# Optimization experiments

Measured on AMD Instinct MI355X. Metric: run time of the kernel, lower is better.

## Reference

```python
import jax, jax.numpy as jnp
import numpy as np

B, P, C = 128, 8732, 21          # batch, num_priors (SSD300), num_classes incl. background
TOP_K = 200
VAR0, VAR1 = 0.1, 0.2            # SSD prior variances
CONF_THRESH = 0.01
NMS_THRESH = 0.45


def setup_inputs() -> dict:
    key = jax.random.key(0)
    k1, k2, k3, k4 = jax.random.split(key, 4)
    loc_data = jax.random.normal(k1, (B, P, 4), jnp.float32)
    conf_data = jax.random.normal(k2, (B * P, C), jnp.float32)
    # priors: (cx, cy, w, h) in [0,1], positive widths/heights
    cxy = jax.random.uniform(k3, (P, 2), jnp.float32)
    wh = jax.random.uniform(k4, (P, 2), jnp.float32, minval=0.02, maxval=0.3)
    prior_data = jnp.concatenate([cxy, wh], axis=-1)
    return {"loc_data": loc_data, "conf_data": conf_data, "prior_data": prior_data}


def _decode(loc, priors):
    # loc: [B,P,4], priors: [P,4] (cx,cy,w,h) -> corner boxes [B,P,4]
    xy = priors[:, :2] + loc[..., :2] * VAR0 * priors[:, 2:]
    wh = priors[:, 2:] * jnp.exp(loc[..., 2:] * VAR1)
    return jnp.concatenate([xy - wh * 0.5, xy + wh * 0.5], axis=-1)


def _nms_single(boxes, scores, idxs):
    # boxes [P,4] corners, scores [P] (-1 where below conf_thresh), idxs [P] int class ids
    x1, y1, x2, y2 = boxes[:, 0], boxes[:, 1], boxes[:, 2], boxes[:, 3]
    areas = (x2 - x1) * (y2 - y1)

    def body(s, _):
        i = jnp.argmax(s)          # highest remaining score
        si = s[i]
        valid = si > 0.0
        bi = boxes[i]
        # IoU of bi against all boxes
        ix1 = jnp.maximum(bi[0], x1)
        iy1 = jnp.maximum(bi[1], y1)
        ix2 = jnp.minimum(bi[2], x2)
        iy2 = jnp.minimum(bi[3], y2)
        inter = jnp.maximum(ix2 - ix1, 0.0) * jnp.maximum(iy2 - iy1, 0.0)
        area_i = (bi[2] - bi[0]) * (bi[3] - bi[1])
        iou = inter / (area_i + areas - inter)
        # class-aware (batched) NMS: only suppress same-class boxes; also kills i itself (iou=1)
        suppress = (iou > NMS_THRESH) & (idxs == idxs[i])
        s_new = jnp.where(suppress, -1.0, s)
        row = jnp.where(
            valid,
            jnp.concatenate([bi, si[None], idxs[i].astype(jnp.float32)[None]]),
            jnp.zeros(6, dtype=boxes.dtype),
        )
        return s_new, row

    _, rows = jax.lax.scan(body, scores, None, length=TOP_K)
    return rows  # [TOP_K, 6] = (x1,y1,x2,y2,score,class)


def reference(loc_data, conf_data, prior_data):
    # softmax over classes, drop background, per-prior best fg class
    conf = jax.nn.softmax(conf_data, axis=-1)[:, 1:].reshape(B, P, C - 1)
    scores = conf.max(axis=-1)           # [B,P]
    cls = jnp.argmax(conf, axis=-1)      # [B,P] fg class id (0..C-2)
    boxes = _decode(loc_data, prior_data)  # [B,P,4]
    masked = jnp.where(scores > CONF_THRESH, scores, -1.0)
    return jax.vmap(_nms_single)(boxes, masked, cls)  # [B, TOP_K, 6]
```

## Files before the change

kernel.cpp:

```cpp
#include <hip/hip_runtime.h>


typedef unsigned long long u64;

#define BATCH 128
#define NPRIOR 8732
#define NCLS 21
#define TOPK 200
#define T 1024
#define TARGET 256
#define CAP 384
#define NBIN 4096
#define KW 6

__device__ __forceinline__ double exp_fast(double x) {
  const double LOG2E = 1.4426950408889634;
  const double LN2_HI = 6.93147180369123816490e-01;
  const double LN2_LO = 1.90821492927058770002e-10;
  double n = rint(x * LOG2E);
  double r = fma(-n, LN2_HI, x);
  r = fma(-n, LN2_LO, r);
  double p = 2.505210838544172e-08;
  p = fma(p, r, 2.755731922398589e-07);
  p = fma(p, r, 2.7557319223985893e-06);
  p = fma(p, r, 2.48015873015873e-05);
  p = fma(p, r, 1.984126984126984e-04);
  p = fma(p, r, 1.388888888888889e-03);
  p = fma(p, r, 8.333333333333333e-03);
  p = fma(p, r, 4.1666666666666664e-02);
  p = fma(p, r, 1.6666666666666666e-01);
  p = fma(p, r, 0.5);
  p = fma(p, r, 1.0);
  p = fma(p, r, 1.0);
  return ldexp(p, (int)n);
}

__global__ __launch_bounds__(256) void prep_kernel(
    const float* __restrict__ conf, u64* __restrict__ keys) {
  __shared__ __align__(16) float srow[256 * NCLS];
  const int tid = threadIdx.x;
  const long long R0 = (long long)blockIdx.x * 256;
  const float4* src = (const float4*)(conf + R0 * NCLS);
  float4* dst = (float4*)srow;
  for (int k = tid; k < 1344; k += 256) dst[k] = src[k];
  __syncthreads();

  const float* row = srow + tid * NCLS;
  float m = row[0];
#pragma unroll
  for (int j = 1; j < NCLS; ++j) m = fmaxf(m, row[j]);
  float sum = __expf(row[0] - m);
  float bestr = row[1];
  float beste = __expf(row[1] - m);
  sum += beste;
  int bi = 1;
#pragma unroll
  for (int j = 2; j < NCLS; ++j) {
    float rv = row[j];
    float ej = __expf(rv - m);
    sum += ej;
    if (rv > bestr) { bestr = rv; bi = j; beste = ej; }
  }
  float score = __fdividef(beste, sum);

  const long long r = R0 + tid;
  const int p = (int)(r % NPRIOR);
  u64 key = 0ULL;
  if (score > 0.01f) {
    key = ((u64)__float_as_uint(score) << 32) |
          ((u64)(16383 - p) << 10) | (u64)(bi - 1);
  }
  keys[r] = key;
}

__device__ __forceinline__ void radix_cut(const int* hist, int tid, int tcap,
                                          int* wtot, int* cut) {
  if (tid == 0) cut[2] = 0;
  const int base = tid * 4;
  const int cs = hist[base] + hist[base + 1] + hist[base + 2] + hist[base + 3];
  const int lane = tid & 63;
  int suf = cs;
#pragma unroll
  for (int off = 1; off < 64; off <<= 1) {
    int v = __shfl_down(suf, off);
    if (lane + off < 64) suf += v;
  }
  if (lane == 0) wtot[tid >> 6] = suf;
  __syncthreads();
  if (tid < 16) {
    int v = wtot[tid];
    int s = v;
#pragma unroll
    for (int off = 1; off < 16; off <<= 1) {
      int o = __shfl_down(s, off);
      if (tid + off < 16) s += o;
    }
    if (tid == 0) wtot[16] = s;
    wtot[tid] = s - v;
  }
  __syncthreads();
  const int total = wtot[16];
  if (total > 0) {
    const int target = total < tcap ? total : tcap;
    const int S = suf + wtot[tid >> 6];
    const int Snext = S - cs;
    if (S >= target && Snext < target) {
      int acc = Snext;
      for (int bn = base + 3; bn >= base; --bn) {
        acc += hist[bn];
        if (acc >= target) {
          cut[0] = bn; cut[1] = acc - hist[bn]; cut[2] = acc;
          break;
        }
      }
    }
  }
  __syncthreads();
}

__global__ __launch_bounds__(T) void nms_kernel(
    const float* __restrict__ loc, const float* __restrict__ conf,
    const float* __restrict__ prior, const u64* __restrict__ keys,
    float* __restrict__ out) {
  __shared__ u64 Ks[NPRIOR];
  __shared__ __align__(16) char pool[53248];
  __shared__ int wtot[17];
  __shared__ int cut1[3], cut2[3];
  __shared__ u64 Ash[KW], KFsh[KW], ACCsh[KW];
  __shared__ float4 abox[TOPK];
  __shared__ float aar[TOPK];
  __shared__ int acl[TOPK];
  __shared__ int sh_cnt, sh_nA;
  __shared__ u64 sh_ub;

  const int tid = threadIdx.x;
  const int b = blockIdx.x;
  const float* confb = conf + (long long)b * (NPRIOR * NCLS);
  const float4* loc4 = ((const float4*)loc) + (long long)b * NPRIOR;
  const float4* pr4 = (const float4*)prior;
  float* outb = out + (long long)b * (TOPK * 6);

  for (int i = tid; i < NPRIOR; i += T) Ks[i] = keys[(long long)b * NPRIOR + i];
  if (tid == 0) { sh_nA = 0; sh_ub = ~0ULL; }
  __syncthreads();

  int* hist = (int*)pool;
  u64* buf = (u64*)(pool + 16384);
  u64* ebuf = (u64*)(pool + 19456);
  u64* buf2 = (u64*)(pool + 22528);
  float4* cbox = (float4*)(pool + 25600);
  float* car = (float*)(pool + 31744);
  int* ccl = (int*)(pool + 33280);
  u64* KILL = (u64*)(pool + 34816);

  while (true) {
    for (int i = tid; i < NBIN; i += T) hist[i] = 0;
    __syncthreads();
    const u64 ub = sh_ub;
    for (int i = tid; i < NPRIOR; i += T) {
      u64 k = Ks[i];
      if (k && k < ub) atomicAdd(&hist[(int)((k >> 46) & 0xFFF)], 1);
    }
    __syncthreads();
    radix_cut(hist, tid, TARGET, wtot, cut1);
    const int total = wtot[16];
    int M = cut1[2];
    if (M == 0) break;
    const int c1 = cut1[0];
    const int baseA = cut1[1];
    const bool need2 = (M > CAP);
    int c2 = 0;
    if (need2) {
      for (int i = tid; i < NBIN; i += T) hist[i] = 0;
      __syncthreads();
      for (int i = tid; i < NPRIOR; i += T) {
        u64 k = Ks[i];
        if (k && k < ub && (int)((k >> 46) & 0xFFF) == c1)
          atomicAdd(&hist[(int)((k >> 34) & 0xFFF)], 1);
      }
      __syncthreads();
      const int tcap2 = (total < TARGET ? total : TARGET) - baseA;
      radix_cut(hist, tid, tcap2, wtot, cut2);
      c2 = cut2[0];
      M = baseA + cut2[2];
      if (M > CAP) {
        int Md = M - hist[c2];
        if (Md > 0) { M = Md; c2 = c2 + 1; } else { M = CAP; }
      }
    }
    if (tid == 0) {
      sh_cnt = 0;
      sh_ub = need2 ? (((u64)c1 << 46) + ((u64)c2 << 34)) : ((u64)c1 << 46);
    }
    __syncthreads();
    for (int i = tid; i < NPRIOR; i += T) {
      u64 k = Ks[i];
      bool psel = false;
      if (k && k < ub) {
        int b1 = (int)((k >> 46) & 0xFFF);
        psel = need2 ? (b1 > c1 || (b1 == c1 && (int)((k >> 34) & 0xFFF) >= c2))
                     : (b1 >= c1);
      }
      u64 mask = __ballot(psel ? 1 : 0);
      if (mask) {
        int lane = tid & 63;
        int leader = __ffsll((unsigned long long)mask) - 1;
        int bpos = 0;
        if (lane == leader) bpos = atomicAdd(&sh_cnt, __popcll(mask));
        bpos = __shfl(bpos, leader);
        if (psel) {
          int pos = bpos + __popcll(mask & ((1ULL << lane) - 1ULL));
          if (pos < CAP) buf[pos] = k;
        }
      }
    }
    __syncthreads();
    int Mr = sh_cnt;
    if (Mr > CAP) Mr = CAP;
    if (Mr == 0) break;
    if (tid < Mr) {
      u64 ak = buf[tid];
      int cl = (int)(ak & 0x1FULL);
      int p = 16383 - (int)((ak >> 10) & 0x3FFFULL);
      const float* crow = confb + (long long)p * NCLS;
      double m = (double)crow[0];
#pragma unroll
      for (int j = 1; j < NCLS; ++j) m = fmax(m, (double)crow[j]);
      double sum = 0.0, best = -1.0;
#pragma unroll
      for (int j = 0; j < NCLS; ++j) {
        double ej = exp_fast((double)crow[j] - m);
        sum += ej;
        if (j >= 1 && ej > best) best = ej;
      }
      double score = best / sum;
      u64 sb = (u64)__double_as_longlong(score);
      ebuf[tid] = ((sb >> 24) << 24) | ((u64)(16383 - p) << 10) | (u64)cl;
    }
    __syncthreads();
    if (tid < Mr) {
      u64 ka = ebuf[tid];
      int ra = 0;
      for (int i = 0; i < Mr; ++i) ra += (ebuf[i] > ka);
      buf2[ra] = ka;
    }
    if (tid < KW) { Ash[tid] = 0ULL; KFsh[tid] = 0ULL; }
    __syncthreads();
    const int nA0 = sh_nA;
    if (tid < Mr) {
      const int t = tid;
      u64 k = buf2[t];
      int cl = (int)(k & 0x1FULL);
      int p = 16383 - (int)((k >> 10) & 0x3FFFULL);
      float4 l = loc4[p];
      float4 pr = pr4[p];
      double cx = (double)pr.x + (double)l.x * 0.1 * (double)pr.z;
      double cy = (double)pr.y + (double)l.y * 0.1 * (double)pr.w;
      double w = (double)pr.z * exp_fast((double)l.z * 0.2);
      double h = (double)pr.w * exp_fast((double)l.w * 0.2);
      float x1 = (float)(cx - w * 0.5), y1 = (float)(cy - h * 0.5);
      float x2 = (float)(cx + w * 0.5), y2 = (float)(cy + h * 0.5);
      cbox[t] = make_float4(x1, y1, x2, y2);
      car[t] = (x2 - x1) * (y2 - y1);
      ccl[t] = cl;
    }
    __syncthreads();
    if (nA0 > 0 && tid < Mr) {
      const int t = tid;
      float4 my = cbox[t];
      float mar = car[t];
      int mcl = ccl[t];
      bool sup = false;
      for (int a = 0; a < nA0; ++a) {
        if (acl[a] == mcl) {
          float4 ab = abox[a];
          float ix1 = fmaxf(ab.x, my.x), iy1 = fmaxf(ab.y, my.y);
          float ix2 = fminf(ab.z, my.z), iy2 = fminf(ab.w, my.w);
          float inter = fmaxf(ix2 - ix1, 0.f) * fmaxf(iy2 - iy1, 0.f);
          if (inter > 0.45f * (aar[a] + mar - inter)) sup = true;
        }
      }
      if (sup) atomicOr(&Ash[t >> 6], 1ULL << (t & 63));
    }
    for (int idx = tid; idx < KW * 512; idx += T) {
      const int seg = idx >> 9;
      const int t = idx & 511;
      if (t < Mr) {
        const int i0 = seg * 64;
        int i1 = i0 + 64;
        if (i1 > Mr) i1 = Mr;
        u64 mm = 0ULL;
        if (i1 > t) {
          float4 my = cbox[t];
          float mar = car[t];
          int mcl = ccl[t];
          int is = (i0 > t + 1) ? i0 : (t + 1);
          for (int i = is; i < i1; ++i) {
            if (ccl[i] == mcl) {
              float4 cb = cbox[i];
              float ix1 = fmaxf(my.x, cb.x), iy1 = fmaxf(my.y, cb.y);
              float ix2 = fminf(my.z, cb.z), iy2 = fminf(my.w, cb.w);
              float inter = fmaxf(ix2 - ix1, 0.f) * fmaxf(iy2 - iy1, 0.f);
              if (inter > 0.45f * (mar + car[i] - inter))
                mm |= 1ULL << (i - i0);
            }
          }
        }
        KILL[t * KW + seg] = mm;
        if (mm) atomicOr(&KFsh[t >> 6], 1ULL << (t & 63));
      }
    }
    __syncthreads();
    if (tid < 64) {
      u64 A0, A1, A2, A3, A4, A5;
      {
        u64 v[KW];
#pragma unroll
        for (int w = 0; w < KW; ++w) {
          int rem = Mr - 64 * w;
          u64 vm = (rem >= 64) ? ~0ULL : (rem <= 0 ? 0ULL : ((1ULL << rem) - 1ULL));
          v[w] = vm & ~Ash[w];
        }
        A0 = v[0]; A1 = v[1]; A2 = v[2]; A3 = v[3]; A4 = v[4]; A5 = v[5];
      }
      u64 C0 = 0, C1 = 0, C2 = 0, C3 = 0, C4 = 0, C5 = 0;
      int nacc = nA0;
      bool full = false;
#define KILLUPD(cidx) do { const u64* kc = &KILL[(cidx) * KW];      \
      A0 &= ~kc[0]; A1 &= ~kc[1]; A2 &= ~kc[2];                     \
      A3 &= ~kc[3]; A4 &= ~kc[4]; A5 &= ~kc[5]; } while (0)
#define RESW(w, Aw, Cw) if (!full) {                                \
      const u64 KFw = KFsh[w];                                      \
      int lim = Mr - (w) * 64; if (lim > 64) lim = 64;              \
      for (int q = 0; q < lim; ++q) {                               \
        if ((Aw >> q) & 1ULL) {                                     \
          Cw |= 1ULL << q; ++nacc;                                  \
          if (nacc == TOPK) { full = true; break; }                 \
          if ((KFw >> q) & 1ULL) KILLUPD((w) * 64 + q);             \
        } } }
      RESW(0, A0, C0)
      RESW(1, A1, C1)
      RESW(2, A2, C2)
      RESW(3, A3, C3)
      RESW(4, A4, C4)
      RESW(5, A5, C5)
#undef RESW
#undef KILLUPD
      if (tid == 0) {
        ACCsh[0] = C0; ACCsh[1] = C1; ACCsh[2] = C2;
        ACCsh[3] = C3; ACCsh[4] = C4; ACCsh[5] = C5;
        sh_nA = nacc;
      }
    }
    __syncthreads();
    if (tid < Mr) {
      const int t = tid;
      const int w = t >> 6, q = t & 63;
      const u64 accw = ACCsh[w];
      if ((accw >> q) & 1ULL) {
        int rank = nA0;
#pragma unroll
        for (int w2 = 0; w2 < KW; ++w2)
          if (w2 < w) rank += __popcll(ACCsh[w2]);
        rank += __popcll(accw & ((q == 0) ? 0ULL : ((1ULL << q) - 1ULL)));
        float4 bx = cbox[t];
        float sc = (float)__longlong_as_double((long long)((buf2[t] >> 24) << 24));
        float* o = outb + rank * 6;
        o[0] = bx.x; o[1] = bx.y; o[2] = bx.z; o[3] = bx.w;
        o[4] = sc; o[5] = (float)ccl[t];
        abox[rank] = bx; aar[rank] = car[t]; acl[rank] = ccl[t];
      }
    }
    __syncthreads();
    if (sh_nA >= TOPK) break;
    if (total - Mr <= 0) break;
  }
  const int nAf = sh_nA;
  for (int i = nAf * 6 + tid; i < TOPK * 6; i += T) outb[i] = 0.0f;
}

extern "C" void kernel_launch(void* const* d_in, const int* in_sizes, int n_in,
                              void* d_out, int out_size, void* d_ws,
                              size_t ws_size, hipStream_t stream) {
  const float* loc = (const float*)d_in[0];
  const float* conf = (const float*)d_in[1];
  const float* prior = (const float*)d_in[2];
  float* out = (float*)d_out;

  u64* keys = (u64*)d_ws;

  const int nrows_blocks = (BATCH * NPRIOR) / 256;
  prep_kernel<<<nrows_blocks, 256, 0, stream>>>(conf, keys);
  nms_kernel<<<BATCH, T, 0, stream>>>(loc, conf, prior, keys, out);
}
```

Before: 211.2 us.

## Micro-optimize NMS kernel: bit-built exp scale, typed LDS arrays, unrolled rank loops

Replaces ldexp in the double exp polynomial with a multiply by a power of two built from raw bits. The untyped shared pool is split into separately typed shared arrays, and conf rows are loaded into registers before the softmax. The rank-by-count loop is unrolled by 8 and the pairwise IoU loop gets an unroll pragma. These target instruction overhead and load latency in the candidate scoring and suppression stages. The bit-built scale has no handling for out-of-range exponents, though the softmax inputs here stay small.

```diff
diff --git a/kernel.cpp b/kernel.cpp
--- a/kernel.cpp
+++ b/kernel.cpp
@@ -32,7 +32,8 @@
   p = fma(p, r, 0.5);
   p = fma(p, r, 1.0);
   p = fma(p, r, 1.0);
-  return ldexp(p, (int)n);
+  double scale = __longlong_as_double(((long long)(1023 + (int)n)) << 52);
+  return p * scale;
 }
 
 __global__ __launch_bounds__(256) void prep_kernel(
@@ -123,7 +124,14 @@
     const float* __restrict__ prior, const u64* __restrict__ keys,
     float* __restrict__ out) {
   __shared__ u64 Ks[NPRIOR];
-  __shared__ __align__(16) char pool[53248];
+  __shared__ int hist[NBIN];
+  __shared__ u64 buf[CAP];
+  __shared__ u64 ebuf[CAP];
+  __shared__ u64 buf2[CAP];
+  __shared__ float4 cbox[CAP];
+  __shared__ float car[CAP];
+  __shared__ int ccl[CAP];
+  __shared__ u64 KILL[CAP * KW];
   __shared__ int wtot[17];
   __shared__ int cut1[3], cut2[3];
   __shared__ u64 Ash[KW], KFsh[KW], ACCsh[KW];
@@ -143,15 +151,6 @@
   for (int i = tid; i < NPRIOR; i += T) Ks[i] = keys[(long long)b * NPRIOR + i];
   if (tid == 0) { sh_nA = 0; sh_ub = ~0ULL; }
   __syncthreads();
-
-  int* hist = (int*)pool;
-  u64* buf = (u64*)(pool + 16384);
-  u64* ebuf = (u64*)(pool + 19456);
-  u64* buf2 = (u64*)(pool + 22528);
-  float4* cbox = (float4*)(pool + 25600);
-  float* car = (float*)(pool + 31744);
-  int* ccl = (int*)(pool + 33280);
-  u64* KILL = (u64*)(pool + 34816);
 
   while (true) {
     for (int i = tid; i < NBIN; i += T) hist[i] = 0;
@@ -223,13 +222,16 @@
       int cl = (int)(ak & 0x1FULL);
       int p = 16383 - (int)((ak >> 10) & 0x3FFFULL);
       const float* crow = confb + (long long)p * NCLS;
-      double m = (double)crow[0];
-#pragma unroll
-      for (int j = 1; j < NCLS; ++j) m = fmax(m, (double)crow[j]);
+      float cr[NCLS];
+#pragma unroll
+      for (int j = 0; j < NCLS; ++j) cr[j] = crow[j];
+      double m = (double)cr[0];
+#pragma unroll
+      for (int j = 1; j < NCLS; ++j) m = fmax(m, (double)cr[j]);
       double sum = 0.0, best = -1.0;
 #pragma unroll
       for (int j = 0; j < NCLS; ++j) {
-        double ej = exp_fast((double)crow[j] - m);
+        double ej = exp_fast((double)cr[j] - m);
         sum += ej;
         if (j >= 1 && ej > best) best = ej;
       }
@@ -241,7 +243,14 @@
     if (tid < Mr) {
       u64 ka = ebuf[tid];
       int ra = 0;
-      for (int i = 0; i < Mr; ++i) ra += (ebuf[i] > ka);
+      int i = 0;
+      for (; i + 8 <= Mr; i += 8) {
+        u64 k0 = ebuf[i], k1 = ebuf[i + 1], k2 = ebuf[i + 2], k3 = ebuf[i + 3];
+        u64 k4 = ebuf[i + 4], k5 = ebuf[i + 5], k6 = ebuf[i + 6], k7 = ebuf[i + 7];
+        ra += (int)(k0 > ka) + (int)(k1 > ka) + (int)(k2 > ka) + (int)(k3 > ka) +
+              (int)(k4 > ka) + (int)(k5 > ka) + (int)(k6 > ka) + (int)(k7 > ka);
+      }
+      for (; i < Mr; ++i) ra += (int)(ebuf[i] > ka);
       buf2[ra] = ka;
     }
     if (tid < KW) { Ash[tid] = 0ULL; KFsh[tid] = 0ULL; }
@@ -295,6 +304,7 @@
           float mar = car[t];
           int mcl = ccl[t];
           int is = (i0 > t + 1) ? i0 : (t + 1);
+#pragma unroll 4
           for (int i = is; i < i1; ++i) {
             if (ccl[i] == mcl) {
               float4 cb = cbox[i];
```

After: 207.0 us. -2.0%, faster.
